# Performance work log

Hardware: AMD Instinct MI355X
Metric: run time of the kernel (lower is better)

The kernel has to match this reference:

```python
import jax, jax.numpy as jnp
import numpy as np

KERNEL_SIZE = 7       # NMS max-pool window
H, W = 512, 1024      # dims
TOP_K = 200
CIRCLE_RADIUS = 5
NUM_CLASSES = 34      # things are labelIds 24..33


def _circle_constants(radius):
    k = 2 * radius + 1
    ii, jj = np.meshgrid(np.arange(k), np.arange(k), indexing='ij')
    ox = (jj - radius).astype(np.float32)  # x offset of neighbor
    oy = (ii - radius).astype(np.float32)  # y offset of neighbor
    cd = np.sqrt(ox ** 2 + oy ** 2)
    cmask = (cd <= radius).astype(np.float32)
    n_pix = float(cmask.sum())
    thr = float((cd * cmask).sum() / n_pix)  # center_threshold buffer
    return ox, oy, cmask, n_pix, thr


def _vote_map(center_regressions, radius):
    # For each pixel p, average over circle neighbors q = p + o of ||o - reg(q)||
    # (get_patches with zero padding), then vote = -avg - 1.
    ox, oy, cmask, n_pix, thr = _circle_constants(radius)
    B, _, h, w = center_regressions.shape
    reg_p = jnp.pad(center_regressions, ((0, 0), (0, 0), (radius, radius), (radius, radius)))
    acc = jnp.zeros((B, h, w), center_regressions.dtype)
    k = 2 * radius + 1
    for i in range(k):          # fixed 11x11 window, ~97 in-circle taps
        for j in range(k):
            if cmask[i, j] == 0.0:
                continue
            rx = reg_p[:, 0, i:i + h, j:j + w]
            ry = reg_p[:, 1, i:i + h, j:j + w]
            acc = acc + jnp.sqrt((ox[i, j] - rx) ** 2 + (oy[i, j] - ry) ** 2)
    vote = -(acc / n_pix) - 1.0  # [B,H,W], always <= -1
    return vote, thr


def _forward(segmentation_logits, center_regressions):
    B = segmentation_logits.shape[0]
    seg_probs = jax.nn.softmax(segmentation_logits, axis=1)                # [B,C,H,W]
    seg_map = jnp.argmax(segmentation_logits, axis=1).astype(jnp.float32)  # [B,H,W]
    # Threshold(23.99, 50) then <= 33  <=>  23.99 < class <= 33
    things = (seg_map > 23.99) & (seg_map <= 33.0)
    # predicted absolute center per pixel; xy_coords are 1-based
    xg = jnp.arange(1, W + 1, dtype=jnp.float32)[None, None, :]
    yg = jnp.arange(1, H + 1, dtype=jnp.float32)[None, :, None]
    px = xg - center_regressions[:, 0]                                     # [B,H,W]
    py = yg - center_regressions[:, 1]
    vote, thr = _vote_map(center_regressions, CIRCLE_RADIUS)
    pooled = jax.lax.reduce_window(vote, -jnp.inf, jax.lax.max,
                                   (1, KERNEL_SIZE, KERNEL_SIZE), (1, 1, 1), 'SAME')
    keep = (pooled == vote) & (vote > -thr - 1.0)
    center_map = jnp.where(keep, vote, 0.0)                                # nms-ed vote map
    # top-k centers: surviving NMS positions ranked by aggregate vote value
    scores = jnp.where(center_map != 0.0, vote, -jnp.inf).reshape(B, -1)
    top_vals, top_idx = jax.lax.top_k(scores, TOP_K)                       # [B,K]
    ys = top_idx // W
    xs = top_idx % W
    valid = jnp.isfinite(top_vals)
    BIG = 1e9
    cx = jnp.where(valid, xs.astype(jnp.float32), BIG)
    cy = jnp.where(valid, ys.astype(jnp.float32), BIG)
    # nearest-center assignment; squared distance (argmin invariant under sqrt)
    d2 = (px[..., None] - cx[:, None, None, :]) ** 2 + (py[..., None] - cy[:, None, None, :]) ** 2
    inst_map = (jnp.argmin(d2, axis=-1).astype(jnp.int32) + 1) * things.astype(jnp.int32)
    return seg_probs, seg_map, center_map, inst_map, ys, xs, top_vals


def _instance_stats(inst_map, seg_map, seg_probs):
    # separate_inst_maps: per instance -> majority seg class, mean prob of that
    # class over the instance mask, and pixel count (vectorized via segment_sum)
    B = inst_map.shape[0]
    seg_ids = seg_map.astype(jnp.int32).reshape(B, -1)                     # [B,HW]
    inst_flat = inst_map.reshape(B, -1)                                    # [B,HW], 0 = background
    onehot = jax.nn.one_hot(seg_ids, NUM_CLASSES, dtype=jnp.float32)       # [B,HW,C]
    probs = jnp.transpose(seg_probs, (0, 2, 3, 1)).reshape(B, -1, NUM_CLASSES)
    seg_counts = jax.vmap(lambda v, s: jax.ops.segment_sum(v, s, num_segments=TOP_K + 1))(onehot, inst_flat)
    prob_sums = jax.vmap(lambda v, s: jax.ops.segment_sum(v, s, num_segments=TOP_K + 1))(probs, inst_flat)
    seg_counts = seg_counts[:, 1:]                                         # drop background -> [B,K,C]
    prob_sums = prob_sums[:, 1:]
    inst_size = seg_counts.sum(-1)                                         # [B,K]
    inst_class = jnp.argmax(seg_counts, axis=-1).astype(jnp.int32)         # [B,K]
    sel = jnp.take_along_axis(prob_sums, inst_class[..., None], axis=-1)[..., 0]
    inst_seg_prob = sel / jnp.maximum(inst_size, 1.0)
    return inst_class, inst_seg_prob, inst_size.astype(jnp.int32)


def setup_inputs() -> dict:
    key = jax.random.key(0)
    k1, k2, k3 = jax.random.split(key, 3)
    return {
        'segmentation_logits': jax.random.normal(k1, (2, NUM_CLASSES, H, W), jnp.float32),
        'center_maps_placeholder': jax.random.normal(k2, (2, 1, H, W), jnp.float32),
        'center_regressions': jax.random.normal(k3, (2, 2, H, W), jnp.float32),
    }


def reference(segmentation_logits, center_maps_placeholder, center_regressions):
    seg_probs, seg_map, center_map, inst_map, ys, xs, top_vals = _forward(
        segmentation_logits, center_regressions)
    inst_class, inst_seg_prob, inst_size = _instance_stats(inst_map, seg_map, seg_probs)
    centers = jnp.stack([ys, xs], -1).astype(jnp.int32)  # (row, col) like torch.nonzero
    return (inst_map, seg_map, centers, top_vals, inst_class, inst_seg_prob, inst_size, center_map)
```

## Files before the change

kernel.cpp:

```cpp
#include <hip/hip_runtime.h>
#include <cfloat>
#include <cmath>

#define NB 2
#define NC 34
#define NH 512
#define NW 1024
#define HWSZ (NH*NW)
#define TK 200
#define CAPC 49152
#define ACH 1024
#define NTH 10
#define ZWORDS (8 + NB*TK*NTH)

#define PST 1040
#define RPROWS 522
#define RPLEFT 8
#define VPROWS 518
#define VPLEFT 4
#define RPSZ (RPROWS*PST)
#define VPSZ (VPROWS*PST)

typedef unsigned long long u64;

#define PREP_ROWB (NB*2*RPROWS)
#define PREP_BR (NB*6)
#define PREP_ST 16
#define PREP_ZB ((ZWORDS + NB*TK + 255)/256 + 1)
__global__ __launch_bounds__(256) void k_prep(const float* __restrict__ reg,
                                              float* __restrict__ reg_pad,
                                              float* __restrict__ vote_pad,
                                              int* __restrict__ zreg,
                                              float* __restrict__ o_iprob) {
    int bid = blockIdx.x;
    int tid = threadIdx.x;
    const float4 NEG4 = make_float4(-INFINITY, -INFINITY, -INFINITY, -INFINITY);
    if (bid < PREP_ROWB) {
        int bc = bid / RPROWS;
        int r = bid % RPROWS;
        float* dst = reg_pad + (size_t)bc * RPSZ + (size_t)r * PST;
        if (r >= 5 && r < 517) {
            const float* src = reg + (size_t)bc * HWSZ + (size_t)(r - 5) * NW;
            *(float4*)(dst + RPLEFT + 4 * tid) = *(const float4*)(src + 4 * tid);
            if (tid < 2) *(float4*)(dst + 4 * tid) = make_float4(0.f, 0.f, 0.f, 0.f);
            else if (tid < 4) *(float4*)(dst + 1032 + 4 * (tid - 2)) = make_float4(0.f, 0.f, 0.f, 0.f);
        } else {
            for (int i = tid; i < PST / 4; i += 256)
                *(float4*)(dst + 4 * i) = make_float4(0.f, 0.f, 0.f, 0.f);
        }
    } else if (bid < PREP_ROWB + PREP_BR) {
        int bid2 = bid - PREP_ROWB;
        int bb = bid2 / 6;
        int rsel = bid2 % 6;
        int r = (rsel < 3) ? rsel : (512 + rsel);
        float* dst = vote_pad + (size_t)bb * VPSZ + (size_t)r * PST;
        for (int i = tid; i < PST / 4; i += 256)
            *(float4*)(dst + 4 * i) = NEG4;
    } else if (bid < PREP_ROWB + PREP_BR + PREP_ST) {
        int idx = (bid - PREP_ROWB - PREP_BR) * 256 + tid;
        int bb = idx >> 11;
        int rem = idx & 2047;
        int r = 3 + (rem >> 2);
        int s = rem & 3;
        int f4 = (s == 0) ? 0 : (256 + s);
        *(float4*)(vote_pad + (size_t)bb * VPSZ + (size_t)r * PST + 4 * f4) = NEG4;
    } else {
        int z = (bid - (PREP_ROWB + PREP_BR + PREP_ST)) * 256 + tid;
        if (z < ZWORDS) zreg[z] = 0;
        else if (z < ZWORDS + NB * TK) o_iprob[z - ZWORDS] = 0.f;
    }
}

#define GETC(f, idx) (((idx)&3)==0 ? f[(idx)>>2].x : ((idx)&3)==1 ? f[(idx)>>2].y : \
                      ((idx)&3)==2 ? f[(idx)>>2].z : f[(idx)>>2].w)

#define VOTEB (NB*NH)
#define SEGB  ((NB*HWSZ)/256)
__global__ __launch_bounds__(256, 4) void k_vote_seg(const float* __restrict__ reg_pad,
                                                     float* __restrict__ vote_pad,
                                                     const float* __restrict__ logits,
                                                     float* __restrict__ segmap_out,
                                                     float* __restrict__ mArr,
                                                     float* __restrict__ dArr) {
    int tid = threadIdx.x;
    int bid = blockIdx.x;
    if (bid >= VOTEB) {
        int p = (bid - VOTEB) * 256 + tid;
        int b = p >> 19;
        int pix = p & (HWSZ - 1);
        const float* basep = logits + (size_t)b * NC * HWSZ + pix;
        float v[NC];
#pragma unroll
        for (int c = 0; c < NC; c++) v[c] = basep[(size_t)c * HWSZ];
        float m = -FLT_MAX; int bc = 0;
#pragma unroll
        for (int c = 0; c < NC; c++) { if (v[c] > m) { m = v[c]; bc = c; } }
        float den = 0.f;
#pragma unroll
        for (int c = 0; c < NC; c++) den += __expf(v[c] - m);
        segmap_out[p] = (float)bc;
        mArr[p] = m;
        dArr[p] = den;
        return;
    }
    int blk = bid;
    int b = blk >> 9;
    int q = blk & 511;
    int y = ((q & 7) << 6) | (q >> 3);
    int xb = tid << 2;
    const float* rp0 = reg_pad + (size_t)(b * 2 + 0) * RPSZ;
    const float* rp1 = reg_pad + (size_t)(b * 2 + 1) * RPSZ;
    float a0 = 0.f, a1 = 0.f, a2 = 0.f, a3 = 0.f;

    float4 fA0[5], fA1[5], fB0[5], fB1[5];

    auto loadwin = [&](int i, float4* f0, float4* f1) {
        const float* p0 = rp0 + (size_t)(y + i) * PST + xb;
        const float* p1 = rp1 + (size_t)(y + i) * PST + xb;
#pragma unroll
        for (int t = 0; t < 5; t++) f0[t] = *(const float4*)(p0 + 4 * t);
#pragma unroll
        for (int t = 0; t < 5; t++) f1[t] = *(const float4*)(p1 + 4 * t);
    };

    auto compute = [&](int i, const float4* f0, const float4* f1) {
        int d = i - 5;
        int ad = d < 0 ? -d : d;
        int w = (int)sqrtf((float)(25 - ad * ad));
        int lo = 5 - w, hi = 5 + w;
        float di = (float)d;
#pragma unroll
        for (int j = 0; j < 11; j++) {
            if (j < lo || j > hi) continue;
            float dj = (float)(j - 5);
            float dx, dy, ss;
            dx = __fsub_rn(dj, GETC(f0, j+3)); dy = __fsub_rn(di, GETC(f1, j+3));
            ss = __fadd_rn(__fmul_rn(dx,dx), __fmul_rn(dy,dy));
            a0 = __fadd_rn(a0, sqrtf(ss));
            dx = __fsub_rn(dj, GETC(f0, j+4)); dy = __fsub_rn(di, GETC(f1, j+4));
            ss = __fadd_rn(__fmul_rn(dx,dx), __fmul_rn(dy,dy));
            a1 = __fadd_rn(a1, sqrtf(ss));
            dx = __fsub_rn(dj, GETC(f0, j+5)); dy = __fsub_rn(di, GETC(f1, j+5));
            ss = __fadd_rn(__fmul_rn(dx,dx), __fmul_rn(dy,dy));
            a2 = __fadd_rn(a2, sqrtf(ss));
            dx = __fsub_rn(dj, GETC(f0, j+6)); dy = __fsub_rn(di, GETC(f1, j+6));
            ss = __fadd_rn(__fmul_rn(dx,dx), __fmul_rn(dy,dy));
            a3 = __fadd_rn(a3, sqrtf(ss));
        }
    };

    loadwin(0, fA0, fA1);
#pragma unroll 1
    for (int i = 0; i < 10; i += 2) {
        loadwin(i + 1, fB0, fB1);
        compute(i, fA0, fA1);
        loadwin(i + 2, fA0, fA1);
        compute(i + 1, fB0, fB1);
    }
    compute(10, fA0, fA1);

    float4 vv;
    vv.x = __fsub_rn(-__fdiv_rn(a0, 81.0f), 1.0f);
    vv.y = __fsub_rn(-__fdiv_rn(a1, 81.0f), 1.0f);
    vv.z = __fsub_rn(-__fdiv_rn(a2, 81.0f), 1.0f);
    vv.w = __fsub_rn(-__fdiv_rn(a3, 81.0f), 1.0f);
    *(float4*)(vote_pad + (size_t)b * VPSZ + (size_t)(y + 3) * PST + (xb + VPLEFT)) = vv;
}

__global__ __launch_bounds__(256) void k_pool(const float* __restrict__ vote_pad,
                                              float* __restrict__ cmap_out,
                                              u64* __restrict__ keys,
                                              int* __restrict__ ccnt,
                                              float thr_keep) {
    int tid = threadIdx.x;
    int blk = blockIdx.x;
    int b = blk >> 9;
    int q = blk & 511;
    int y = ((q & 7) << 6) | (q >> 3);
    int xb = tid << 2;
    const float* vp = vote_pad + (size_t)b * VPSZ;
    float cm[10];
#pragma unroll
    for (int t = 0; t < 10; t++) cm[t] = -INFINITY;
    float vv[4];
#pragma unroll 1
    for (int dy = -3; dy <= 3; dy++) {
        const float* row = vp + (size_t)(y + dy + 3) * PST + xb;
        float4 A = *(const float4*)(row);
        float4 Bq = *(const float4*)(row + 4);
        float4 Cq = *(const float4*)(row + 8);
        float L[12] = {A.x,A.y,A.z,A.w, Bq.x,Bq.y,Bq.z,Bq.w, Cq.x,Cq.y,Cq.z,Cq.w};
#pragma unroll
        for (int t = 0; t < 10; t++) cm[t] = fmaxf(cm[t], L[t + 1]);
        if (dy == 0) { vv[0]=L[4]; vv[1]=L[5]; vv[2]=L[6]; vv[3]=L[7]; }
    }
    int pix = y * NW + xb;
    float cmap[4];
#pragma unroll
    for (int k = 0; k < 4; k++) {
        float mx = cm[k];
#pragma unroll
        for (int u = 1; u < 7; u++) mx = fmaxf(mx, cm[k+u]);
        bool keep = (mx == vv[k]) && (vv[k] > thr_keep);
        cmap[k] = keep ? vv[k] : 0.0f;
        if (keep) {
            int pos = atomicAdd(&ccnt[b], 1);
            if (pos < CAPC) {
                unsigned u = __float_as_uint(vv[k]);
                unsigned ou = ((int)u < 0) ? ~u : (u | 0x80000000u);
                keys[(size_t)b * CAPC + pos] = ((u64)ou << 19) | (u64)(HWSZ - 1 - (pix + k));
            }
        }
    }
    *(float4*)(cmap_out + b * HWSZ + pix) = make_float4(cmap[0],cmap[1],cmap[2],cmap[3]);
}

__device__ inline void bitonic_desc(u64* a, int np2, int tid, int T) {
    for (int k = 2; k <= np2; k <<= 1) {
        for (int j = k >> 1; j > 0; j >>= 1) {
            for (int i = tid; i < np2; i += T) {
                int ixj = i ^ j;
                if (ixj > i) {
                    u64 x = a[i], y = a[ixj];
                    bool up = ((i & k) == 0);
                    if (up ? (x < y) : (x > y)) { a[i] = y; a[ixj] = x; }
                }
            }
            __syncthreads();
        }
    }
}

__global__ __launch_bounds__(1024) void k_topk(const u64* __restrict__ keys_g,
                                               const int* __restrict__ ccnt,
                                               float* __restrict__ cxArr,
                                               float* __restrict__ cyArr,
                                               float* __restrict__ out_centers,
                                               float* __restrict__ out_topvals) {
    __shared__ int hist[2048];
    __shared__ int ssum[1024];
    __shared__ u64 sel[256];
    __shared__ int scnt;
    __shared__ int sB, sSab, scB;
    const int T = 1024;
    int b = blockIdx.x;
    int tid = threadIdx.x;
    int n = ccnt[b];
    if (n > CAPC) n = CAPC;
    const u64* Kg = keys_g + (size_t)b * CAPC;

    u64 thr;
    if (n <= TK) {
        thr = 1;
    } else {
        u64 prefixval = 0;
        int pbits = 0, need = TK;
        thr = 0;
        const int widths[5] = {11, 11, 11, 11, 7};
        bool done = false;
        for (int lvl = 0; lvl < 5 && !done; ++lvl) {
            int w = widths[lvl];
            int nb = 1 << w;
            int shift = 51 - pbits - w;
            for (int i = tid; i < nb; i += T) hist[i] = 0;
            __syncthreads();
            for (int i = tid; i < n; i += T) {
                u64 k = Kg[i];
                if ((k >> (51 - pbits)) == prefixval)
                    atomicAdd(&hist[(int)((k >> shift) & (u64)(nb - 1))], 1);
            }
            __syncthreads();
            int items = (nb + T - 1) / T;
            int sv = 0;
            for (int it = 0; it < items; ++it) {
                int j = tid * items + it;
                if (j < nb) sv += hist[j];
            }
            ssum[tid] = sv;
            __syncthreads();
            for (int off = 1; off < T; off <<= 1) {
                int v = (tid + off < T) ? ssum[tid + off] : 0;
                __syncthreads();
                ssum[tid] += v;
                __syncthreads();
            }
            int incl = ssum[tid];
            int excl = (tid + 1 < T) ? ssum[tid + 1] : 0;
            if (excl < need && need <= incl) {
                int acc = excl;
                int base2 = tid * items;
                for (int it = items - 1; it >= 0; --it) {
                    int j = base2 + it;
                    if (j >= nb) continue;
                    int h = hist[j];
                    if (acc + h >= need) { sB = j; sSab = acc; scB = h; break; }
                    acc += h;
                }
            }
            __syncthreads();
            int B = sB, Sab = sSab, cB = scB;
            int sel_total = (TK - need) + Sab;
            if (sel_total + cB <= 256) {
                thr = ((prefixval << w) | (u64)B) << shift;
                done = true;
            } else {
                prefixval = (prefixval << w) | (u64)B;
                pbits += w;
                need = need - Sab;
            }
            __syncthreads();
        }
    }

    if (tid == 0) scnt = 0;
    if (tid < 256) sel[tid] = 0;
    __syncthreads();
    for (int i = tid; i < n; i += T) {
        u64 k = Kg[i];
        if (k >= thr && k != 0ULL) {
            int p = atomicAdd(&scnt, 1);
            if (p < 256) sel[p] = k;
        }
    }
    __syncthreads();
    bitonic_desc(sel, 256, tid, T);
    if (tid < TK) {
        u64 w = sel[tid];
        bool valid = (w != 0ULL);
        unsigned ou = (unsigned)(w >> 19);
        unsigned ub = (ou & 0x80000000u) ? (ou & 0x7FFFFFFFu) : ~ou;
        float v = __uint_as_float(ub);
        int pix = valid ? (int)(HWSZ - 1 - (int)(w & 0x7FFFFULL)) : 0x7fffffff;
        int ys = pix >> 10;
        int xs = pix & (NW - 1);
        cxArr[b * TK + tid] = valid ? (float)xs : 1e9f;
        cyArr[b * TK + tid] = valid ? (float)ys : 1e9f;
        out_centers[(b * TK + tid) * 2 + 0] = (float)ys;
        out_centers[(b * TK + tid) * 2 + 1] = (float)xs;
        out_topvals[b * TK + tid] = valid ? v : -INFINITY;
    }
}

__global__ __launch_bounds__(256) void k_assign(const float* __restrict__ reg,
                                                const float* __restrict__ segmap,
                                                const float* __restrict__ cxArr,
                                                const float* __restrict__ cyArr,
                                                float* __restrict__ out_inst,
                                                int* __restrict__ segcnt) {
    __shared__ int lcnt[TK * NTH];
    __shared__ float swx[TK];
    __shared__ float swy[TK];
    __shared__ int swk[TK];
    __shared__ float sred[256];
    __shared__ int wcnt[4];
    __shared__ float sbox[4];

    int tid = threadIdx.x;
    int bid = blockIdx.x;
    int b = bid >> 9;
    int r = bid & 511;
    int ty = r >> 5, tx = r & 31;
    int y0 = ty << 5, x0 = tx << 5;
    int row = tid >> 3;
    int col = (tid & 7) << 2;
    int y = y0 + row;
    int x = x0 + col;
    int pix0 = (y << 10) + x;

    for (int t = tid; t < TK * NTH; t += 256) lcnt[t] = 0;

    const float* r0 = reg + (size_t)b * 2 * HWSZ;
    const float* r1 = r0 + HWSZ;
    float4 rx = *(const float4*)(r0 + pix0);
    float4 ry = *(const float4*)(r1 + pix0);
    float px[4], py[4];
    px[0] = __fsub_rn((float)(x + 1), rx.x); py[0] = __fsub_rn((float)(y + 1), ry.x);
    px[1] = __fsub_rn((float)(x + 2), rx.y); py[1] = __fsub_rn((float)(y + 1), ry.y);
    px[2] = __fsub_rn((float)(x + 3), rx.z); py[2] = __fsub_rn((float)(y + 1), ry.z);
    px[3] = __fsub_rn((float)(x + 4), rx.w); py[3] = __fsub_rn((float)(y + 1), ry.w);

    float pxlo = fminf(fminf(px[0], px[1]), fminf(px[2], px[3]));
    float pxhi = fmaxf(fmaxf(px[0], px[1]), fmaxf(px[2], px[3]));
    float pylo = fminf(fminf(py[0], py[1]), fminf(py[2], py[3]));
    float pyhi = fmaxf(fmaxf(py[0], py[1]), fmaxf(py[2], py[3]));
#pragma unroll
    for (int off = 32; off >= 1; off >>= 1) {
        pxlo = fminf(pxlo, __shfl_xor(pxlo, off));
        pxhi = fmaxf(pxhi, __shfl_xor(pxhi, off));
        pylo = fminf(pylo, __shfl_xor(pylo, off));
        pyhi = fmaxf(pyhi, __shfl_xor(pyhi, off));
    }
    int wid = tid >> 6;
    int lane = tid & 63;
    if (lane == 0) {
        sred[wid * 4 + 0] = pxlo; sred[wid * 4 + 1] = pxhi;
        sred[wid * 4 + 2] = pylo; sred[wid * 4 + 3] = pyhi;
    }
    __syncthreads();
    if (tid == 0) {
        float a = sred[0], bq = sred[1], c = sred[2], d = sred[3];
        for (int w = 1; w < 4; w++) {
            a  = fminf(a,  sred[w * 4 + 0]);
            bq = fmaxf(bq, sred[w * 4 + 1]);
            c  = fminf(c,  sred[w * 4 + 2]);
            d  = fmaxf(d,  sred[w * 4 + 3]);
        }
        sbox[0] = a; sbox[1] = bq; sbox[2] = c; sbox[3] = d;
    }
    __syncthreads();
    float bxlo = sbox[0], bxhi = sbox[1], bylo = sbox[2], byhi = sbox[3];

    float Lk = 0.f, Uk = INFINITY, cxv = 0.f, cyv = 0.f;
    if (tid < TK) {
        cxv = cxArr[b * TK + tid];
        cyv = cyArr[b * TK + tid];
        float dl = fmaxf(fmaxf(__fsub_rn(bxlo, cxv), __fsub_rn(cxv, bxhi)), 0.f);
        float el = fmaxf(fmaxf(__fsub_rn(bylo, cyv), __fsub_rn(cyv, byhi)), 0.f);
        float du = fmaxf(__fsub_rn(cxv, bxlo), __fsub_rn(bxhi, cxv));
        float eu = fmaxf(__fsub_rn(cyv, bylo), __fsub_rn(byhi, cyv));
        Lk = __fadd_rn(__fmul_rn(dl, dl), __fmul_rn(el, el));
        Uk = __fadd_rn(__fmul_rn(du, du), __fmul_rn(eu, eu));
    }
    sred[tid] = Uk;
    __syncthreads();
#pragma unroll
    for (int s = 128; s > 0; s >>= 1) {
        if (tid < s) sred[tid] = fminf(sred[tid], sred[tid + s]);
        __syncthreads();
    }
    float Umin = sred[0];

    bool flag = (tid < TK) && (Lk <= Umin);
    u64 mask = __ballot(flag);
    int wpre = __popcll(mask & ((1ULL << lane) - 1ULL));
    if (lane == 0) wcnt[wid] = (int)__popcll(mask);
    __syncthreads();
    int base_off = 0;
#pragma unroll
    for (int w = 0; w < 4; w++) if (w < wid) base_off += wcnt[w];
    int m = wcnt[0] + wcnt[1] + wcnt[2] + wcnt[3];
    if (flag) {
        int p = base_off + wpre;
        swx[p] = cxv; swy[p] = cyv; swk[p] = tid;
    }
    __syncthreads();

    float bd[4]; int bk[4];
#pragma unroll
    for (int it = 0; it < 4; it++) { bd[it] = INFINITY; bk[it] = 0; }
    for (int k2 = 0; k2 < m; k2++) {
        float cx = swx[k2];
        float cy = swy[k2];
        int kk = swk[k2];
#pragma unroll
        for (int it = 0; it < 4; it++) {
            float dx = __fsub_rn(px[it], cx);
            float dy = __fsub_rn(py[it], cy);
            float d2 = __fadd_rn(__fmul_rn(dx, dx), __fmul_rn(dy, dy));
            if (d2 < bd[it]) { bd[it] = d2; bk[it] = kk; }
        }
    }

    float4 sm = *(const float4*)(segmap + (size_t)b * HWSZ + pix0);
    float scls[4] = {sm.x, sm.y, sm.z, sm.w};
    float oi[4];
#pragma unroll
    for (int it = 0; it < 4; it++) {
        int cls = (int)scls[it];
        int thing = (cls >= 24) ? 1 : 0;
        int inst = (bk[it] + 1) * thing;
        oi[it] = (float)inst;
        if (inst) atomicAdd(&lcnt[bk[it] * NTH + (cls - 24)], 1);
    }
    *(float4*)(out_inst + (size_t)b * HWSZ + pix0) = make_float4(oi[0], oi[1], oi[2], oi[3]);
    __syncthreads();
    for (int t = tid; t < TK * NTH; t += 256) {
        int v = lcnt[t];
        if (v) atomicAdd(&segcnt[b * TK * NTH + t], v);
    }
}

__global__ __launch_bounds__(256) void k_statsprob(const float* __restrict__ logits,
                                                   const float* __restrict__ inst_f,
                                                   const float* __restrict__ mArr,
                                                   const float* __restrict__ dArr,
                                                   const int* __restrict__ segcnt,
                                                   float* __restrict__ out_icls,
                                                   float* __restrict__ out_isize,
                                                   float* __restrict__ out_iprob) {
    __shared__ float lps[TK];
    __shared__ int sicls[TK];
    __shared__ float ssz[TK];
    int tid = threadIdx.x;
    int base = blockIdx.x * ACH;
    int b = base >> 19;
    if (tid < TK) {
        const int* rowp = segcnt + (size_t)(b * TK + tid) * NTH;
        int total = 0, bc = 0, bv = -1;
#pragma unroll
        for (int c = 0; c < NTH; c++) {
            int v = rowp[c];
            total += v;
            if (v > bv) { bv = v; bc = c; }
        }
        int cls = (total == 0) ? 0 : (24 + bc);
        sicls[tid] = cls;
        ssz[tid] = fmaxf((float)total, 1.0f);
        if ((blockIdx.x & 511) == 0) {
            out_icls[b * TK + tid] = (float)cls;
            out_isize[b * TK + tid] = (float)total;
        }
    }
    for (int t = tid; t < TK; t += 256) lps[t] = 0.f;
    __syncthreads();
    int p0 = base + tid * 4;
    float4 fi = *(const float4*)(inst_f + p0);
    float4 fm = *(const float4*)(mArr + p0);
    float4 fd = *(const float4*)(dArr + p0);
    float insts[4] = {fi.x, fi.y, fi.z, fi.w};
    float ms[4] = {fm.x, fm.y, fm.z, fm.w};
    float ds[4] = {fd.x, fd.y, fd.z, fd.w};
#pragma unroll
    for (int it = 0; it < 4; it++) {
        int inst = (int)insts[it];
        if (inst) {
            int p = p0 + it;
            int pix = p & (HWSZ - 1);
            int c = sicls[inst - 1];
            float xv = logits[(size_t)(b * NC + c) * HWSZ + pix];
            float pr = __fdiv_rn(__expf(__fsub_rn(xv, ms[it])), ds[it]);
            atomicAdd(&lps[inst - 1], pr);
        }
    }
    __syncthreads();
    for (int t = tid; t < TK; t += 256) {
        float s = lps[t];
        if (s != 0.f) {
            float sz = ssz[t];
            atomicAdd(&out_iprob[b * TK + t], s / sz);
        }
    }
}

static float compute_thr_keep() {
    float cdm[121];
    int t = 0;
    for (int i = 0; i < 11; i++) {
        for (int j = 0; j < 11; j++) {
            float ox = (float)(j - 5), oy = (float)(i - 5);
            float cd = sqrtf(ox * ox + oy * oy);
            float cm = (cd <= 5.0f) ? 1.0f : 0.0f;
            cdm[t++] = cd * cm;
        }
    }
    float r[8];
    for (int k = 0; k < 8; k++) r[k] = cdm[k];
    int i = 8;
    for (; i < 121 - (121 % 8); i += 8)
        for (int k = 0; k < 8; k++) r[k] += cdm[i + k];
    float res = ((r[0] + r[1]) + (r[2] + r[3])) + ((r[4] + r[5]) + (r[6] + r[7]));
    for (; i < 121; i++) res += cdm[i];
    float thr = res / 81.0f;
    double kt = -(double)thr - 1.0;
    return (float)kt;
}

extern "C" void kernel_launch(void* const* d_in, const int* in_sizes, int n_in,
                              void* d_out, int out_size, void* d_ws, size_t ws_size,
                              hipStream_t stream) {
    const float* logits = (const float*)d_in[0];
    const float* reg    = (const float*)d_in[2];
    float* out = (float*)d_out;

    float* o_inst    = out;
    float* o_seg     = out + 1048576;
    float* o_centers = out + 2097152;
    float* o_topvals = out + 2097952;
    float* o_icls    = out + 2098352;
    float* o_iprob   = out + 2098752;
    float* o_isize   = out + 2099152;
    float* o_cmap    = out + 2099552;

    u64* keys = (u64*)d_ws;
    float* wsf = (float*)(keys + (size_t)NB * CAPC);
    size_t o = 0;
    int*   zreg    = (int*)(wsf + o); o += ZWORDS;
    int*   ccnt    = zreg;
    int*   segcnt  = zreg + 8;
    float* reg_pad = wsf + o; o += (size_t)NB * 2 * RPSZ;
    float* vote_pad= wsf + o; o += (size_t)NB * VPSZ;
    float* mArr    = wsf + o; o += (size_t)NB * HWSZ;
    float* dArr    = wsf + o; o += (size_t)NB * HWSZ;
    float* cxArr   = wsf + o; o += NB * TK;
    float* cyArr   = wsf + o; o += NB * TK;

    float thr_keep = compute_thr_keep();

    int gridPrep = PREP_ROWB + PREP_BR + PREP_ST + PREP_ZB;
    int gridVS = VOTEB + SEGB;
    int gridRow = NB * NH;
    int gridAgg = (NB * HWSZ) / ACH;

    k_prep<<<gridPrep, 256, 0, stream>>>(reg, reg_pad, vote_pad, zreg, o_iprob);
    k_vote_seg<<<gridVS, 256, 0, stream>>>(reg_pad, vote_pad, logits, o_seg, mArr, dArr);
    k_pool<<<gridRow, 256, 0, stream>>>(vote_pad, o_cmap, keys, ccnt, thr_keep);
    k_topk<<<NB, 1024, 0, stream>>>(keys, ccnt, cxArr, cyArr, o_centers, o_topvals);
    k_assign<<<gridAgg, 256, 0, stream>>>(reg, o_seg, cxArr, cyArr, o_inst, segcnt);
    k_statsprob<<<gridAgg, 256, 0, stream>>>(logits, o_inst, mArr, dArr, segcnt, o_icls, o_isize, o_iprob);
}
```

Measured before the change: 341.4 us.

## Drop padded regression copy and fold prep work into vote kernel

Removes the k_prep kernel that copied center regressions into a zero-padded buffer. The vote kernel now reads the original regressions directly, using bounds checks for the border rows and edge threads. The -inf border fills and workspace zeroing are moved into extra blocks of the vote/seg launch. This saves one kernel launch and about 8 MB of copy traffic, at the cost of branchy, scalar loads at image borders.

```diff
diff --git a/kernel.cpp b/kernel.cpp
--- a/kernel.cpp
+++ b/kernel.cpp
@@ -14,76 +14,57 @@
 #define ZWORDS (8 + NB*TK*NTH)
 
 #define PST 1040
-#define RPROWS 522
-#define RPLEFT 8
 #define VPROWS 518
 #define VPLEFT 4
-#define RPSZ (RPROWS*PST)
 #define VPSZ (VPROWS*PST)
 
 typedef unsigned long long u64;
 
-#define PREP_ROWB (NB*2*RPROWS)
-#define PREP_BR (NB*6)
-#define PREP_ST 16
-#define PREP_ZB ((ZWORDS + NB*TK + 255)/256 + 1)
-__global__ __launch_bounds__(256) void k_prep(const float* __restrict__ reg,
-                                              float* __restrict__ reg_pad,
-                                              float* __restrict__ vote_pad,
-                                              int* __restrict__ zreg,
-                                              float* __restrict__ o_iprob) {
-    int bid = blockIdx.x;
-    int tid = threadIdx.x;
-    const float4 NEG4 = make_float4(-INFINITY, -INFINITY, -INFINITY, -INFINITY);
-    if (bid < PREP_ROWB) {
-        int bc = bid / RPROWS;
-        int r = bid % RPROWS;
-        float* dst = reg_pad + (size_t)bc * RPSZ + (size_t)r * PST;
-        if (r >= 5 && r < 517) {
-            const float* src = reg + (size_t)bc * HWSZ + (size_t)(r - 5) * NW;
-            *(float4*)(dst + RPLEFT + 4 * tid) = *(const float4*)(src + 4 * tid);
-            if (tid < 2) *(float4*)(dst + 4 * tid) = make_float4(0.f, 0.f, 0.f, 0.f);
-            else if (tid < 4) *(float4*)(dst + 1032 + 4 * (tid - 2)) = make_float4(0.f, 0.f, 0.f, 0.f);
-        } else {
-            for (int i = tid; i < PST / 4; i += 256)
-                *(float4*)(dst + 4 * i) = make_float4(0.f, 0.f, 0.f, 0.f);
-        }
-    } else if (bid < PREP_ROWB + PREP_BR) {
-        int bid2 = bid - PREP_ROWB;
-        int bb = bid2 / 6;
-        int rsel = bid2 % 6;
-        int r = (rsel < 3) ? rsel : (512 + rsel);
-        float* dst = vote_pad + (size_t)bb * VPSZ + (size_t)r * PST;
-        for (int i = tid; i < PST / 4; i += 256)
-            *(float4*)(dst + 4 * i) = NEG4;
-    } else if (bid < PREP_ROWB + PREP_BR + PREP_ST) {
-        int idx = (bid - PREP_ROWB - PREP_BR) * 256 + tid;
-        int bb = idx >> 11;
-        int rem = idx & 2047;
-        int r = 3 + (rem >> 2);
-        int s = rem & 3;
-        int f4 = (s == 0) ? 0 : (256 + s);
-        *(float4*)(vote_pad + (size_t)bb * VPSZ + (size_t)r * PST + 4 * f4) = NEG4;
-    } else {
-        int z = (bid - (PREP_ROWB + PREP_BR + PREP_ST)) * 256 + tid;
-        if (z < ZWORDS) zreg[z] = 0;
-        else if (z < ZWORDS + NB * TK) o_iprob[z - ZWORDS] = 0.f;
-    }
-}
+#define VOTEB (NB*NH)
+#define SEGB  ((NB*HWSZ)/256)
+#define AUX_BR (NB*6)
+#define AUX_ST 16
+#define AUX_ZB ((ZWORDS + NB*TK + 255)/256 + 1)
+#define AUXB (AUX_BR + AUX_ST + AUX_ZB)
 
 #define GETC(f, idx) (((idx)&3)==0 ? f[(idx)>>2].x : ((idx)&3)==1 ? f[(idx)>>2].y : \
                       ((idx)&3)==2 ? f[(idx)>>2].z : f[(idx)>>2].w)
 
-#define VOTEB (NB*NH)
-#define SEGB  ((NB*HWSZ)/256)
-__global__ __launch_bounds__(256, 4) void k_vote_seg(const float* __restrict__ reg_pad,
+__global__ __launch_bounds__(256, 4) void k_vote_seg(const float* __restrict__ reg,
                                                      float* __restrict__ vote_pad,
                                                      const float* __restrict__ logits,
                                                      float* __restrict__ segmap_out,
                                                      float* __restrict__ mArr,
-                                                     float* __restrict__ dArr) {
+                                                     float* __restrict__ dArr,
+                                                     int* __restrict__ zreg,
+                                                     float* __restrict__ o_iprob) {
     int tid = threadIdx.x;
     int bid = blockIdx.x;
+    if (bid >= VOTEB + SEGB) {
+        int a = bid - (VOTEB + SEGB);
+        const float4 NEG4 = make_float4(-INFINITY, -INFINITY, -INFINITY, -INFINITY);
+        if (a < AUX_BR) {
+            int bb = a / 6;
+            int rsel = a % 6;
+            int r = (rsel < 3) ? rsel : (512 + rsel);
+            float* dst = vote_pad + (size_t)bb * VPSZ + (size_t)r * PST;
+            for (int i = tid; i < PST / 4; i += 256)
+                *(float4*)(dst + 4 * i) = NEG4;
+        } else if (a < AUX_BR + AUX_ST) {
+            int idx = (a - AUX_BR) * 256 + tid;
+            int bb = idx >> 11;
+            int rem = idx & 2047;
+            int r = 3 + (rem >> 2);
+            int s = rem & 3;
+            int f4 = (s == 0) ? 0 : (256 + s);
+            *(float4*)(vote_pad + (size_t)bb * VPSZ + (size_t)r * PST + 4 * f4) = NEG4;
+        } else {
+            int z = (a - AUX_BR - AUX_ST) * 256 + tid;
+            if (z < ZWORDS) zreg[z] = 0;
+            else if (z < ZWORDS + NB * TK) o_iprob[z - ZWORDS] = 0.f;
+        }
+        return;
+    }
     if (bid >= VOTEB) {
         int p = (bid - VOTEB) * 256 + tid;
         int b = p >> 19;
@@ -108,19 +89,44 @@
     int q = blk & 511;
     int y = ((q & 7) << 6) | (q >> 3);
     int xb = tid << 2;
-    const float* rp0 = reg_pad + (size_t)(b * 2 + 0) * RPSZ;
-    const float* rp1 = reg_pad + (size_t)(b * 2 + 1) * RPSZ;
+    const float* reg0 = reg + (size_t)(b * 2 + 0) * HWSZ;
+    const float* reg1 = reg + (size_t)(b * 2 + 1) * HWSZ;
     float a0 = 0.f, a1 = 0.f, a2 = 0.f, a3 = 0.f;
 
     float4 fA0[5], fA1[5], fB0[5], fB1[5];
 
     auto loadwin = [&](int i, float4* f0, float4* f1) {
-        const float* p0 = rp0 + (size_t)(y + i) * PST + xb;
-        const float* p1 = rp1 + (size_t)(y + i) * PST + xb;
-#pragma unroll
-        for (int t = 0; t < 5; t++) f0[t] = *(const float4*)(p0 + 4 * t);
-#pragma unroll
-        for (int t = 0; t < 5; t++) f1[t] = *(const float4*)(p1 + 4 * t);
+        int r = y + i - 5;
+        if (r >= 0 && r < NH) {
+            const float* p0 = reg0 + (size_t)r * NW + (xb - 8);
+            const float* p1 = reg1 + (size_t)r * NW + (xb - 8);
+            if (tid >= 2 && tid < 254) {
+#pragma unroll
+                for (int t = 0; t < 5; t++) f0[t] = *(const float4*)(p0 + 4 * t);
+#pragma unroll
+                for (int t = 0; t < 5; t++) f1[t] = *(const float4*)(p1 + 4 * t);
+            } else {
+#pragma unroll
+                for (int t = 0; t < 5; t++) {
+                    float e0[4], e1[4];
+#pragma unroll
+                    for (int e = 0; e < 4; e++) {
+                        int c = xb - 8 + 4 * t + e;
+                        bool ok = (c >= 0) && (c < NW);
+                        e0[e] = ok ? reg0[(size_t)r * NW + c] : 0.f;
+                        e1[e] = ok ? reg1[(size_t)r * NW + c] : 0.f;
+                    }
+                    f0[t] = make_float4(e0[0], e0[1], e0[2], e0[3]);
+                    f1[t] = make_float4(e1[0], e1[1], e1[2], e1[3]);
+                }
+            }
+        } else {
+#pragma unroll
+            for (int t = 0; t < 5; t++) {
+                f0[t] = make_float4(0.f, 0.f, 0.f, 0.f);
+                f1[t] = make_float4(0.f, 0.f, 0.f, 0.f);
+            }
+        }
     };
 
     auto compute = [&](int i, const float4* f0, const float4* f1) {
@@ -587,7 +593,6 @@
     int*   zreg    = (int*)(wsf + o); o += ZWORDS;
     int*   ccnt    = zreg;
     int*   segcnt  = zreg + 8;
-    float* reg_pad = wsf + o; o += (size_t)NB * 2 * RPSZ;
     float* vote_pad= wsf + o; o += (size_t)NB * VPSZ;
     float* mArr    = wsf + o; o += (size_t)NB * HWSZ;
     float* dArr    = wsf + o; o += (size_t)NB * HWSZ;
@@ -596,13 +601,11 @@
 
     float thr_keep = compute_thr_keep();
 
-    int gridPrep = PREP_ROWB + PREP_BR + PREP_ST + PREP_ZB;
-    int gridVS = VOTEB + SEGB;
+    int gridVS = VOTEB + SEGB + AUXB;
     int gridRow = NB * NH;
     int gridAgg = (NB * HWSZ) / ACH;
 
-    k_prep<<<gridPrep, 256, 0, stream>>>(reg, reg_pad, vote_pad, zreg, o_iprob);
-    k_vote_seg<<<gridVS, 256, 0, stream>>>(reg_pad, vote_pad, logits, o_seg, mArr, dArr);
+    k_vote_seg<<<gridVS, 256, 0, stream>>>(reg, vote_pad, logits, o_seg, mArr, dArr, zreg, o_iprob);
     k_pool<<<gridRow, 256, 0, stream>>>(vote_pad, o_cmap, keys, ccnt, thr_keep);
     k_topk<<<NB, 1024, 0, stream>>>(keys, ccnt, cxArr, cyArr, o_centers, o_topvals);
     k_assign<<<gridAgg, 256, 0, stream>>>(reg, o_seg, cxArr, cyArr, o_inst, segcnt);
```

After: 348.8 us. 2.2% more time.
